# Optimization experiments

Measured on AMD Instinct MI355X. Metric: run time of the kernel, lower is better.

The kernel has to match this reference:

```python
import jax, jax.numpy as jnp
import numpy as np

N, B, C, T, IN_DIM, L, RANK, OUT_DIM = 2000, 16, 32, 12, 2, 3, 4, 1
CN = C // 4  # channel_num = 8
EPS = 1e-5


def _adj_month():
    a = np.diag(np.ones(12)) / 3.0
    np.fill_diagonal(a[1:], 1.0 / 3.0)
    np.fill_diagonal(a[:, 1:], 1.0 / 3.0)
    a[0, 11] = 1.0 / 3.0
    a[11, 0] = 1.0 / 3.0
    return jnp.asarray(a, dtype=jnp.float32)


def _circ_conv(xb, w, b, k):
    # xb: [B,N,C,T]; w: [N,CN,C,k]; b: [N,CN]  ->  [B,N,CN,T]
    # Circular pad on the right by k-1 (matches F.pad(...,(0,k-1)) mode='circular').
    Tt = xb.shape[-1]
    xp = jnp.concatenate([xb, xb[..., :k - 1]], axis=-1)          # [B,N,C,T+k-1]
    win = jnp.stack([xp[..., j:j + Tt] for j in range(k)], axis=-1)  # [B,N,C,T,k]
    return jnp.einsum('bnctk,nock->bnot', win, w) + b[None, :, :, None]


def setup_inputs() -> dict:
    key = jax.random.key(0)
    ks = jax.random.split(key, 32)

    def rn(i, shape, scale=0.05):
        return jax.random.normal(ks[i], shape, dtype=jnp.float32) * scale

    D_cw = CN * C * 18 * L   # 13824
    D_cb = CN * 4 * L        # 96
    D_rw = C * C * L         # 3072
    D_rb = C * L             # 96

    inp = jax.random.normal(ks[0], (B, IN_DIM, N, T + 1), dtype=jnp.float32)
    inp = inp.at[0, 0, 0, -1].set(5.0)  # valid month index
    adj = jax.random.uniform(ks[1], (N, N), dtype=jnp.float32) / N

    return dict(
        input=inp, adj=adj,
        characteristics=rn(2, (N, 12, RANK), 0.5),
        W_convw=rn(3, (RANK, D_cw)), b_convw=rn(4, (D_cw,)),
        W_convb=rn(5, (RANK, D_cb)), b_convb=rn(6, (D_cb,)),
        W_gatew=rn(7, (RANK, D_cw)), b_gatew=rn(8, (D_cw,)),
        W_gateb=rn(9, (RANK, D_cb)), b_gateb=rn(10, (D_cb,)),
        W_resw=rn(11, (RANK, D_rw)), b_resw=rn(12, (D_rw,)),
        W_resb=rn(13, (RANK, D_rb)), b_resb=rn(14, (D_rb,)),
        start_w=rn(15, (C, IN_DIM), 0.5), start_b=rn(16, (C,)),
        skip0_w=rn(17, (C, IN_DIM, T), 0.2), skip0_b=rn(18, (C,)),
        skip_w=rn(19, (L, C, T), 0.2), skip_b=rn(20, (L, C)),
        skipE_w=rn(21, (C, T), 0.2), skipE_b=rn(22, (C,)),
        ln_w=jnp.ones((L, C, N, T), jnp.float32),
        ln_b=jnp.zeros((L, C, N, T), jnp.float32),
        end1_w=rn(23, (C, C), 0.2), end1_b=rn(24, (C,)),
        end2_w=rn(25, (OUT_DIM, C), 0.2), end2_b=rn(26, (OUT_DIM,)),
    )


def reference(input, adj, characteristics, W_convw, b_convw, W_convb, b_convb,
              W_gatew, b_gatew, W_gateb, b_gateb, W_resw, b_resw, W_resb, b_resb,
              start_w, start_b, skip0_w, skip0_b, skip_w, skip_b, skipE_w, skipE_b,
              ln_w, ln_b, end1_w, end1_b, end2_w, end2_b):
    # month index from last time slot (eval mode: dropout = identity)
    month = jnp.mod(input[0, 0, 0, -1].astype(jnp.int32), 12)
    x_in = input[..., :T]                                   # [B,IN,N,T]

    am = _adj_month()                                       # [12,12]
    char = jnp.einsum('ms,nsr->nmr', am, characteristics)   # [N,12,R]
    char_m = jnp.take(char, month, axis=1)                  # [N,R]
    ch = adj @ char_m                                       # graph aggregation [N,R]

    cw_all = ch @ W_convw + b_convw                         # [N, CN*C*18*L]
    cb_all = ch @ W_convb + b_convb                         # [N, CN*4*L]
    gw_all = ch @ W_gatew + b_gatew
    gb_all = ch @ W_gateb + b_gateb
    rw_all = ch @ W_resw + b_resw                           # [N, C*C*L]
    rb_all = ch @ W_resb + b_resb                           # [N, C*L]

    x = jnp.einsum('bint,ci->bcnt', x_in, start_w) + start_b[None, :, None, None]
    skip = jnp.einsum('bint,cit->bcn', x_in, skip0_w) + skip0_b[None, :, None]  # [B,C,N]

    pw = CN * C                                             # 256
    # (kernel slice lo, hi, width) per multiscale branch
    slices = [(0, 2, 2), (2, 5, 3), (5, 11, 6), (11, 18, 7)]
    q = N * CN

    for i in range(L):
        residual = x
        cw = cw_all[:, i * 18 * pw:(i + 1) * 18 * pw].reshape(N, CN, C, 18)
        gw = gw_all[:, i * 18 * pw:(i + 1) * 18 * pw].reshape(N, CN, C, 18)
        # NOTE: torch flattens bias node-major THEN slices quarters -> reproduces
        # the original (node-mixing) bias indexing exactly.
        cb_flat = cb_all[:, i * 4 * CN:(i + 1) * 4 * CN].reshape(-1)   # [N*4*CN]
        gb_flat = gb_all[:, i * 4 * CN:(i + 1) * 4 * CN].reshape(-1)

        xb = jnp.transpose(x, (0, 2, 1, 3))                 # [B,N,C,T]
        f_segs, g_segs = [], []
        for s, (lo, hi, k) in enumerate(slices):
            f = _circ_conv(xb, cw[..., lo:hi], cb_flat[s * q:(s + 1) * q].reshape(N, CN), k)
            g = _circ_conv(xb, gw[..., lo:hi], gb_flat[s * q:(s + 1) * q].reshape(N, CN), k)
            f_segs.append(jnp.transpose(f, (0, 2, 1, 3)))   # [B,CN,N,T]
            g_segs.append(jnp.transpose(g, (0, 2, 1, 3)))
        filt = jnp.tanh(jnp.concatenate(f_segs, axis=1))    # [B,C,N,T]
        gate = jax.nn.sigmoid(jnp.concatenate(g_segs, axis=1))
        x = filt * gate

        s_out = jnp.einsum('bcnt,ct->bcn', x, skip_w[i]) + skip_b[i][None, :, None]
        skip = s_out + skip

        rw = rw_all[:, i * C * C:(i + 1) * C * C].reshape(N, C, C)   # [N,out,in]
        rb = rb_all[:, i * C:(i + 1) * C]                            # [N,C]
        xr = jnp.einsum('bnct,noc->bnot', jnp.transpose(x, (0, 2, 1, 3)), rw) \
             + rb[None, :, :, None]
        x = jnp.transpose(xr, (0, 2, 1, 3)) + residual

        # LayerNorm over all non-batch dims (C,N,T) with affine params
        mu = jnp.mean(x, axis=(1, 2, 3), keepdims=True)
        var = jnp.mean(jnp.square(x - mu), axis=(1, 2, 3), keepdims=True)
        x = (x - mu) / jnp.sqrt(var + EPS) * ln_w[i][None] + ln_b[i][None]

    sE = jnp.einsum('bcnt,ct->bcn', x, skipE_w) + skipE_b[None, :, None]
    skip = jax.nn.relu(sE + skip)                           # [B,C,N]
    y = jax.nn.relu(jnp.einsum('bcn,oc->bon', skip, end1_w) + end1_b[None, :, None])
    y = jnp.einsum('bcn,oc->bon', y, end2_w) + end2_b[None, :, None]
    return y[..., None]                                     # [B,OUT_DIM,N,1]
```

## Files before the change

kernel.cpp:

```cpp
#include <hip/hip_runtime.h>

#define NN 2000
#define TT 12

#define XOFF    0
#define SKOFF   6144000
#define CHOFF   7168000
#define CMOFF   7176000
#define STOFF   7184000
#define PARTOFF 7184100
#define PKWOFF  7248100
#define PKBOFF  7358692
#define PKROFF  7386340

typedef __fp16 f16x8 __attribute__((ext_vector_type(8)));
typedef __fp16 h2    __attribute__((ext_vector_type(2)));
typedef float  f32x4 __attribute__((ext_vector_type(4)));

union U32H2 { unsigned int u; __fp16 h[2]; h2 v; };
__device__ __forceinline__ unsigned int pkh(float a, float b){
  U32H2 x; x.h[0] = (__fp16)a; x.h[1] = (__fp16)b; return x.u;
}
__device__ __forceinline__ h2 u2h(unsigned int u){ U32H2 x; x.u = u; return x.v; }
__device__ __forceinline__ unsigned int h2u(h2 v){ U32H2 x; x.v = v; return x.u; }
__device__ __forceinline__ float fsig(float x){ return 1.0f/(1.0f + __expf(-x)); }
__device__ __forceinline__ float ftanh(float x){ return 1.0f - 2.0f/(1.0f + __expf(2.0f*x)); }

__global__ void k_charm(const float* __restrict__ input,
                        const float* __restrict__ charac,
                        float* __restrict__ cm)
{
  int idx = blockIdx.x*256 + threadIdx.x;
  if (idx >= NN*4) return;
  int n = idx >> 2, r = idx & 3;
  int mv = (int)input[TT];
  int m = ((mv % 12) + 12) % 12;
  int m0 = (m + 11) % 12, m2 = (m + 1) % 12;
  const float* base = charac + n*48;
  cm[idx] = (base[m0*4+r] + base[m*4+r] + base[m2*4+r]) * (1.0f/3.0f);
}

__global__ __launch_bounds__(256) void k_ch(const float* __restrict__ adj,
                                            const float* __restrict__ cm,
                                            float* __restrict__ ch)
{
  __shared__ float red[256][4];
  int n = blockIdx.x, t = threadIdx.x;
  float s0=0.f, s1=0.f, s2=0.f, s3=0.f;
  const float* arow = adj + (size_t)n*NN;
  for (int c = t; c < NN; c += 256){
    float a = arow[c];
    float4 v = *reinterpret_cast<const float4*>(cm + c*4);
    s0 = fmaf(a, v.x, s0); s1 = fmaf(a, v.y, s1);
    s2 = fmaf(a, v.z, s2); s3 = fmaf(a, v.w, s3);
  }
  red[t][0]=s0; red[t][1]=s1; red[t][2]=s2; red[t][3]=s3;
  __syncthreads();
  for (int off = 128; off > 0; off >>= 1){
    if (t < off){
      red[t][0]+=red[t+off][0]; red[t][1]+=red[t+off][1];
      red[t][2]+=red[t+off][2]; red[t][3]+=red[t+off][3];
    }
    __syncthreads();
  }
  if (t < 4) ch[n*4+t] = red[0][t];
}

__global__ __launch_bounds__(256) void k_prep(
    const float* __restrict__ Wcw, const float* __restrict__ bcw,
    const float* __restrict__ Wgw, const float* __restrict__ bgw,
    const float* __restrict__ Wrw, const float* __restrict__ brw,
    float* __restrict__ PKW, float* __restrict__ PKB, float* __restrict__ PKR)
{
  int col = blockIdx.x*256 + threadIdx.x;
  if (col < 13824){
    int layer = col / 4608;
    int i     = col - layer*4608;
    int o     = i / 576;
    int rem   = i - o*576;
    int c     = rem / 18;
    int u     = rem - c*18;
    size_t j  = (size_t)layer*4608 + o*576 + u*32 + c;
    float4 a = make_float4(Wcw[col], Wcw[13824+col], Wcw[27648+col], Wcw[41472+col]);
    float4 b = make_float4(Wgw[col], Wgw[13824+col], Wgw[27648+col], Wgw[41472+col]);
    *reinterpret_cast<float4*>(PKW + j*8)     = a;
    *reinterpret_cast<float4*>(PKW + j*8 + 4) = b;
    *reinterpret_cast<float2*>(PKB + j*2) = make_float2(bcw[col], bgw[col]);
  }
  if (col < 3072){
    float4 r = make_float4(Wrw[col], Wrw[3072+col], Wrw[6144+col], Wrw[9216+col]);
    *reinterpret_cast<float4*>(PKR + (size_t)col*8) = r;
    PKR[(size_t)col*8 + 4] = brw[col];
  }
}

__global__ __launch_bounds__(256) void k_stats(
    int layer, const float* __restrict__ parts, float* __restrict__ stats)
{
  __shared__ float red[256];
  const int j = blockIdx.x, tid = threadIdx.x;
  float s = 0.f;
  for (int i = tid; i < NN; i += 256) s += parts[(size_t)i*32 + j];
  red[tid] = s;
  __syncthreads();
  for (int off = 128; off > 0; off >>= 1){
    if (tid < off) red[tid] += red[tid+off];
    __syncthreads();
  }
  if (tid == 0) stats[layer*32 + j] = red[0];
}

__global__ __launch_bounds__(256,3) void k_layer(
    int layer,
    __fp16* __restrict__ xbuf, float* __restrict__ skipbuf,
    const float* __restrict__ ch, const float* __restrict__ stats,
    float* __restrict__ parts,
    const float* __restrict__ input,
    const float* __restrict__ PKW, const float* __restrict__ PKB,
    const float* __restrict__ PKR,
    const float* __restrict__ Wcb, const float* __restrict__ bcb,
    const float* __restrict__ Wgb, const float* __restrict__ bgb,
    const float* __restrict__ Wrb, const float* __restrict__ brb,
    const float* __restrict__ start_w, const float* __restrict__ start_b,
    const float* __restrict__ sk0w, const float* __restrict__ sk0b,
    const float* __restrict__ skw_all, const float* __restrict__ skb_all,
    const float* __restrict__ lnw_all, const float* __restrict__ lnb_all)
{
  __shared__ __fp16 AhG[10752];
  __shared__ __fp16 xh[7680];
  __shared__ __fp16 rwh[1280];
  __shared__ float skred[1024];
  __shared__ float wred[128];
  __shared__ float ubuf[1280];
  __shared__ float skwv[384];
  __shared__ float skbv[32], fbias[32], gbias[32], rbv[32];
  __shared__ float muv[16], rsv[16];

  const int tid = threadIdx.x;
  const int n = blockIdx.x;

  float* swv  = ubuf;
  float* sbv  = ubuf + 64;
  float* s0wv = ubuf + 96;
  float* s0bv = ubuf + 864;
  float* xin  = ubuf + 896;
  __fp16* lnh = reinterpret_cast<__fp16*>(ubuf);

  const float c0v = ch[n*4+0], c1v = ch[n*4+1], c2v = ch[n*4+2], c3v = ch[n*4+3];

  for (int i = tid; i < 32; i += 256) skbv[i] = skb_all[layer*32+i];
  for (int i = tid; i < 384; i += 256) skwv[i] = skw_all[layer*384+i];
  if (layer == 0){
    for (int i = tid; i < 64; i += 256) swv[i] = start_w[i];
    for (int i = tid; i < 32; i += 256){ sbv[i] = start_b[i]; s0bv[i] = sk0b[i]; }
    for (int i = tid; i < 768; i += 256) s0wv[i] = sk0w[i];
    for (int i = tid; i < 384; i += 256){
      int bb = i/24, r = i%24, d = r/12, t = r%12;
      xin[i] = input[(((size_t)bb*2 + d)*NN + n)*13 + t];
    }
  } else {
    for (int i = tid; i < 384; i += 256){
      int c = i/12, t = i%12;
      size_t o = (((size_t)(layer-1)*32 + c)*NN + n)*12 + t;
      lnh[t*32+c]       = (__fp16)lnw_all[o];
      lnh[384 + t*32+c] = (__fp16)lnb_all[o];
    }
    if (tid < 16){
      float S1 = stats[(layer-1)*32 + tid];
      float S2 = stats[(layer-1)*32 + 16 + tid];
      const float M = 768000.0f;
      float mu = S1 / M;
      muv[tid] = mu;
      rsv[tid] = rsqrtf(S2/M - mu*mu + 1e-5f);
    }
  }

  {
    const int cc = tid & 31;
    const int o  = tid >> 5;
    const int o104 = o*104, o232 = o*232;
    const float* pw  = PKW + (size_t)layer*4608*8 + ((size_t)o*576 + cc)*8;
    const float* pbp = PKB + (size_t)layer*4608*2 + ((size_t)o*576 + cc)*2;
#pragma unroll
    for (int u = 0; u < 18; ++u){
      const int s    = (u >= 2) + (u >= 5) + (u >= 11);
      const int lo   = (s == 0) ? 0 : ((s == 1) ? 2 : ((s == 2) ? 5 : 11));
      const int jj   = u - lo;
      const int strd = (s >= 2) ? 232 : 104;
      const int base = ((s >= 2) ? 3328 : 0) + ((s & 1) << 3)*strd + jj*32;
      const int ooff = (s >= 2) ? o232 : o104;
      float4 pwf = *reinterpret_cast<const float4*>(pw + (size_t)u*256);
      float4 pwg = *reinterpret_cast<const float4*>(pw + (size_t)u*256 + 4);
      float2 pb  = *reinterpret_cast<const float2*>(pbp + (size_t)u*64);
      float wf = fmaf(c0v, pwf.x, fmaf(c1v, pwf.y,
                 fmaf(c2v, pwf.z, fmaf(c3v, pwf.w, pb.x))));
      float wg = fmaf(c0v, pwg.x, fmaf(c1v, pwg.y,
                 fmaf(c2v, pwg.z, fmaf(c3v, pwg.w, pb.y))));
      AhG[base + ooff + cc]             = (__fp16)wf;
      AhG[base + ooff + cc + 16*strd]   = (__fp16)wg;
    }
  }
  for (int i = tid; i < 1024; i += 256){
    int grp = i >> 8, rem = i & 255, r = rem >> 5, c = rem & 31;
    int base = (grp < 2) ? 0 : 3328;
    int strd = (grp < 2) ? 104 : 232;
    int off  = (grp < 2) ? 64 : 192;
    int gofs = (grp & 1) ? 16*strd : 0;
    AhG[base + gofs + r*strd + off + c] = (__fp16)0.f;
  }
  for (int i = tid; i < 1024; i += 256){
    int col = layer*1024 + i;
    float4 pr = *reinterpret_cast<const float4*>(PKR + (size_t)col*8);
    float rb = PKR[(size_t)col*8 + 4];
    float v = fmaf(c0v, pr.x, fmaf(c1v, pr.y,
              fmaf(c2v, pr.z, fmaf(c3v, pr.w, rb))));
    rwh[(i>>5)*40 + (i&31)] = (__fp16)v;
  }
  if (tid < 32){
    int oc = tid;
    int s = oc >> 3;
    int v = ((n&3)<<3) + (oc&7);
    int col = layer*32 + v;
    float cb0 = ch[(s*500 + (n>>2))*4 + 0];
    float cb1 = ch[(s*500 + (n>>2))*4 + 1];
    float cb2 = ch[(s*500 + (n>>2))*4 + 2];
    float cb3 = ch[(s*500 + (n>>2))*4 + 3];
    fbias[oc] = fmaf(cb0, Wcb[col], fmaf(cb1, Wcb[96+col],
                fmaf(cb2, Wcb[192+col], fmaf(cb3, Wcb[288+col], bcb[col]))));
    gbias[oc] = fmaf(cb0, Wgb[col], fmaf(cb1, Wgb[96+col],
                fmaf(cb2, Wgb[192+col], fmaf(cb3, Wgb[288+col], bgb[col]))));
    int colr = layer*32 + oc;
    rbv[oc] = fmaf(c0v, Wrb[colr], fmaf(c1v, Wrb[96+colr],
              fmaf(c2v, Wrb[192+colr], fmaf(c3v, Wrb[288+colr], brb[colr]))));
  }
  __syncthreads();

  if (tid < 192){
    int b = tid & 15, t = tid >> 4;
    unsigned int pk[16];
    if (layer == 0){
      float xa = xin[b*24 + t], xb2 = xin[b*24 + 12 + t];
      float xv[32];
#pragma unroll
      for (int c = 0; c < 32; ++c)
        xv[c] = fmaf(swv[c*2], xa, fmaf(swv[c*2+1], xb2, sbv[c]));
#pragma unroll
      for (int j = 0; j < 16; ++j) pk[j] = pkh(xv[2*j], xv[2*j+1]);
    } else {
      const uint4* src = reinterpret_cast<const uint4*>(
          xbuf + (((size_t)b*NN + n)*12 + t)*32);
      uint4 u0 = src[0], u1 = src[1], u2 = src[2], u3 = src[3];
      unsigned int uu[16] = {u0.x,u0.y,u0.z,u0.w, u1.x,u1.y,u1.z,u1.w,
                             u2.x,u2.y,u2.z,u2.w, u3.x,u3.y,u3.z,u3.w};
      __fp16 muh = (__fp16)muv[b], rsh = (__fp16)rsv[b];
      h2 mu2; mu2.x = muh; mu2.y = muh;
      h2 rs2; rs2.x = rsh; rs2.y = rsh;
      const h2* lnw2 = reinterpret_cast<const h2*>(lnh + t*32);
      const h2* lnb2 = reinterpret_cast<const h2*>(lnh + 384 + t*32);
#pragma unroll
      for (int j = 0; j < 16; ++j){
        h2 v = u2h(uu[j]);
        h2 r = (v - mu2) * rs2;
        h2 x2 = r * lnw2[j] + lnb2[j];
        pk[j] = h2u(x2);
      }
    }
    uint4* dst = reinterpret_cast<uint4*>(&xh[(t*16 + b)*40]);
    dst[0] = make_uint4(pk[0], pk[1], pk[2], pk[3]);
    dst[1] = make_uint4(pk[4], pk[5], pk[6], pk[7]);
    dst[2] = make_uint4(pk[8], pk[9], pk[10], pk[11]);
    dst[3] = make_uint4(pk[12],pk[13],pk[14],pk[15]);
  }
  __syncthreads();

  const int lane = tid & 63, w = tid >> 6;
  const int h = w & 1, nh = w >> 1;
  const int r16 = lane & 15, hi4 = lane >> 4;
  const int c0 = hi4*8;
  const int oc0 = h*16 + hi4*4;

  const __fp16* Ab = AhG + (h ? 3328 : 0);
  const int As  = h ? 232 : 104;
  const int njj = h ? 7 : 3;
  f16x8 aF[7], aG[7];
#pragma unroll 7
  for (int jj = 0; jj < 7; ++jj) if (jj < njj){
    aF[jj] = *reinterpret_cast<const f16x8*>(&Ab[r16*As + jj*32 + c0]);
    aG[jj] = *reinterpret_cast<const f16x8*>(&Ab[(16 + r16)*As + jj*32 + c0]);
  }
  f16x8 ar = *reinterpret_cast<const f16x8*>(&rwh[(h*16 + r16)*40 + c0]);
  float fb4[4], gb4[4], rb4[4];
#pragma unroll
  for (int i2 = 0; i2 < 4; ++i2){
    fb4[i2] = fbias[oc0+i2]; gb4[i2] = gbias[oc0+i2]; rb4[i2] = rbv[oc0+i2];
  }
  __syncthreads();
  __fp16* gh = AhG;

  float sv[4] = {0.f, 0.f, 0.f, 0.f};
#pragma unroll
  for (int q = 0; q < 6; ++q){
    int nt = nh*6 + q;
    f32x4 accf = {0.f,0.f,0.f,0.f}, accg = {0.f,0.f,0.f,0.f};
#pragma unroll 7
    for (int jj = 0; jj < 7; ++jj) if (jj < njj){
      int tp = nt + jj; if (tp >= 12) tp -= 12;
      f16x8 bf = *reinterpret_cast<const f16x8*>(&xh[(tp*16 + r16)*40 + c0]);
      accf = __builtin_amdgcn_mfma_f32_16x16x32_f16(aF[jj], bf, accf, 0, 0, 0);
      accg = __builtin_amdgcn_mfma_f32_16x16x32_f16(aG[jj], bf, accg, 0, 0, 0);
    }
    float gv4[4];
#pragma unroll
    for (int i2 = 0; i2 < 4; ++i2){
      float fv = ftanh(accf[i2] + fb4[i2]);
      float gg = fsig(accg[i2] + gb4[i2]);
      gv4[i2] = fv * gg;
      sv[i2] = fmaf(gv4[i2], skwv[(oc0+i2)*12 + nt], sv[i2]);
    }
    *reinterpret_cast<uint2*>(&gh[(nt*16 + r16)*40 + oc0]) =
        make_uint2(pkh(gv4[0], gv4[1]), pkh(gv4[2], gv4[3]));
  }
#pragma unroll
  for (int i2 = 0; i2 < 4; ++i2)
    skred[((oc0+i2)*16 + r16)*2 + nh] = sv[i2];
  __syncthreads();

  for (int e = tid; e < 512; e += 256){
    int b = e >> 5, oc = e & 31;
    float sk = skred[(oc*16+b)*2] + skred[(oc*16+b)*2+1] + skbv[oc];
    size_t so = ((size_t)b*NN + n)*32 + oc;
    if (layer == 0){
      float s0 = s0bv[oc];
#pragma unroll
      for (int r = 0; r < 24; ++r) s0 = fmaf(xin[b*24+r], s0wv[oc*24+r], s0);
      skipbuf[so] = sk + s0;
    } else {
      skipbuf[so] += sk;
    }
  }
  {
    float s1 = 0.f, s2 = 0.f;
#pragma unroll
    for (int q = 0; q < 6; ++q){
      int nt = nh*6 + q;
      f16x8 bg = *reinterpret_cast<const f16x8*>(&gh[(nt*16 + r16)*40 + c0]);
      f32x4 z = {0.f,0.f,0.f,0.f};
      f32x4 acc = __builtin_amdgcn_mfma_f32_16x16x32_f16(ar, bg, z, 0, 0, 0);
      uint2 xu = *reinterpret_cast<const uint2*>(&xh[(nt*16 + r16)*40 + oc0]);
      U32H2 ua, ub; ua.u = xu.x; ub.u = xu.y;
      float o0 = acc[0] + rb4[0] + (float)ua.h[0];
      float o1 = acc[1] + rb4[1] + (float)ua.h[1];
      float o2 = acc[2] + rb4[2] + (float)ub.h[0];
      float o3 = acc[3] + rb4[3] + (float)ub.h[1];
      *reinterpret_cast<uint2*>(
          xbuf + (((size_t)r16*NN + n)*12 + nt)*32 + oc0) =
          make_uint2(pkh(o0, o1), pkh(o2, o3));
      s1 += o0 + o1 + o2 + o3;
      s2 = fmaf(o0,o0, fmaf(o1,o1, fmaf(o2,o2, fmaf(o3,o3, s2))));
    }
    s1 += __shfl_xor(s1, 16); s2 += __shfl_xor(s2, 16);
    s1 += __shfl_xor(s1, 32); s2 += __shfl_xor(s2, 32);
    if (hi4 == 0){
      wred[(w*16 + r16)*2]     = s1;
      wred[(w*16 + r16)*2 + 1] = s2;
    }
  }
  __syncthreads();
  if (tid < 16){
    float a1 = 0.f, a2 = 0.f;
    for (int w2 = 0; w2 < 4; ++w2){
      a1 += wred[(w2*16 + tid)*2];
      a2 += wred[(w2*16 + tid)*2 + 1];
    }
    parts[(size_t)n*32 + tid]      = a1;
    parts[(size_t)n*32 + 16 + tid] = a2;
  }
}

__global__ __launch_bounds__(256) void k_final(
    const __fp16* __restrict__ xbuf, const float* __restrict__ skipbuf,
    const float* __restrict__ stats,
    const float* __restrict__ lnw_all, const float* __restrict__ lnb_all,
    const float* __restrict__ skEw, const float* __restrict__ skEb,
    const float* __restrict__ e1w, const float* __restrict__ e1b,
    const float* __restrict__ e2w, const float* __restrict__ e2b,
    float* __restrict__ out)
{
  __shared__ float lnw[384], lnb[384], skE[384];
  __shared__ float e1[32*33];
  __shared__ float e1bv[32], e2v[32], skEbv[32];
  __shared__ float muv[16], rsv[16];
  __shared__ float skf[8][33];
  const int tid = threadIdx.x, n = blockIdx.x;
  for (int i = tid; i < 384; i += 256){
    int c = i/12, t = i%12;
    size_t o = (((size_t)2*32 + c)*NN + n)*12 + t;
    lnw[i] = lnw_all[o]; lnb[i] = lnb_all[o];
    skE[i] = skEw[i];
  }
  for (int i = tid; i < 1024; i += 256) e1[(i>>5)*33 + (i&31)] = e1w[i];
  if (tid < 32){ e1bv[tid] = e1b[tid]; e2v[tid] = e2w[tid]; skEbv[tid] = skEb[tid]; }
  if (tid < 16){
    float S1 = stats[64+tid], S2 = stats[80+tid];
    const float M = 768000.0f;
    float mu = S1/M; muv[tid] = mu;
    rsv[tid] = rsqrtf(S2/M - mu*mu + 1e-5f);
  }
  __syncthreads();
  const float e2b0 = e2b[0];
  for (int bo = 0; bo < 2; ++bo){
    const int g = tid >> 5, c = tid & 31, b = bo*8 + g;
    float xr[12];
#pragma unroll
    for (int t = 0; t < 12; ++t)
      xr[t] = (float)xbuf[(((size_t)b*NN + n)*12 + t)*32 + c];
    const float mu = muv[b], rs = rsv[b];
    float se = 0.0f;
#pragma unroll
    for (int t = 0; t < 12; ++t){
      float xv = fmaf((xr[t]-mu)*rs, lnw[c*12+t], lnb[c*12+t]);
      se = fmaf(xv, skE[c*12+t], se);
    }
    float sk = se + skEbv[c] + skipbuf[((size_t)b*NN+n)*32 + c];
    skf[g][c] = fmaxf(sk, 0.0f);
    __syncthreads();
    float acc = e1bv[c];
#pragma unroll
    for (int cc = 0; cc < 32; ++cc) acc = fmaf(skf[g][cc], e1[c*33+cc], acc);
    float y1 = fmaxf(acc, 0.0f);
    float part = y1 * e2v[c];
#pragma unroll
    for (int off = 16; off > 0; off >>= 1) part += __shfl_down(part, off, 32);
    if (c == 0) out[(size_t)b*NN + n] = part + e2b0;
    __syncthreads();
  }
}

extern "C" void kernel_launch(void* const* d_in, const int* in_sizes, int n_in,
                              void* d_out, int out_size, void* d_ws, size_t ws_size,
                              hipStream_t stream)
{
  (void)in_sizes; (void)n_in; (void)out_size; (void)ws_size;
  const float* input   = (const float*)d_in[0];
  const float* adj     = (const float*)d_in[1];
  const float* charac  = (const float*)d_in[2];
  const float* Wcw     = (const float*)d_in[3];
  const float* bcw     = (const float*)d_in[4];
  const float* Wcb     = (const float*)d_in[5];
  const float* bcb     = (const float*)d_in[6];
  const float* Wgw     = (const float*)d_in[7];
  const float* bgw     = (const float*)d_in[8];
  const float* Wgb     = (const float*)d_in[9];
  const float* bgb     = (const float*)d_in[10];
  const float* Wrw     = (const float*)d_in[11];
  const float* brw     = (const float*)d_in[12];
  const float* Wrb     = (const float*)d_in[13];
  const float* brb     = (const float*)d_in[14];
  const float* start_w = (const float*)d_in[15];
  const float* start_b = (const float*)d_in[16];
  const float* sk0w    = (const float*)d_in[17];
  const float* sk0b    = (const float*)d_in[18];
  const float* skw     = (const float*)d_in[19];
  const float* skb     = (const float*)d_in[20];
  const float* skEw    = (const float*)d_in[21];
  const float* skEb    = (const float*)d_in[22];
  const float* lnw     = (const float*)d_in[23];
  const float* lnb     = (const float*)d_in[24];
  const float* e1w     = (const float*)d_in[25];
  const float* e1b     = (const float*)d_in[26];
  const float* e2w     = (const float*)d_in[27];
  const float* e2b     = (const float*)d_in[28];

  float* ws     = (float*)d_ws;
  __fp16* xbuf  = (__fp16*)(ws + XOFF);
  float* skipb  = ws + SKOFF;
  float* chbuf  = ws + CHOFF;
  float* cmbuf  = ws + CMOFF;
  float* stats  = ws + STOFF;
  float* parts  = ws + PARTOFF;
  float* PKW    = ws + PKWOFF;
  float* PKB    = ws + PKBOFF;
  float* PKR    = ws + PKROFF;
  float* outp   = (float*)d_out;

  k_prep<<<54, 256, 0, stream>>>(Wcw, bcw, Wgw, bgw, Wrw, brw, PKW, PKB, PKR);
  k_charm<<<32, 256, 0, stream>>>(input, charac, cmbuf);
  k_ch<<<NN, 256, 0, stream>>>(adj, cmbuf, chbuf);
  for (int layer = 0; layer < 3; ++layer){
    k_layer<<<NN, 256, 0, stream>>>(layer, xbuf, skipb, chbuf, stats, parts, input,
        PKW, PKB, PKR, Wcb, bcb, Wgb, bgb, Wrb, brb,
        start_w, start_b, sk0w, sk0b, skw, skb, lnw, lnb);
    k_stats<<<32, 256, 0, stream>>>(layer, parts, stats);
  }
  k_final<<<NN, 256, 0, stream>>>(xbuf, skipb, stats, lnw, lnb,
      skEw, skEb, e1w, e1b, e2w, e2b, outp);
}
```

Measured before the change: 192.2 us.

## Shrink k_layer LDS footprint and template on layer 0 for higher occupancy

Templates k_layer on whether it is layer 0, so layers 1-2 use a smaller shared buffer and a launch bound of 4 blocks per CU instead of 3. LDS is cut further by storing skip weights, biases and skip partial sums as fp16, aliasing skip-reduction and wred scratch into the AhG buffer, and tightening the xh/gh row pitch from 40 to 36 halves with 8-byte loads. The goal is more resident blocks per CU to hide latency. The trade-offs are extra fp16 rounding on biases and skip sums, possible LDS bank conflicts from the new pitch, and narrower loads.

```diff
diff --git a/kernel.cpp b/kernel.cpp
--- a/kernel.cpp
+++ b/kernel.cpp
@@ -18,6 +18,7 @@
 typedef float  f32x4 __attribute__((ext_vector_type(4)));
 
 union U32H2 { unsigned int u; __fp16 h[2]; h2 v; };
+union U2X8  { struct { uint2 a, b; } p; f16x8 v; };
 __device__ __forceinline__ unsigned int pkh(float a, float b){
   U32H2 x; x.h[0] = (__fp16)a; x.h[1] = (__fp16)b; return x.u;
 }
@@ -110,7 +111,8 @@
   if (tid == 0) stats[layer*32 + j] = red[0];
 }
 
-__global__ __launch_bounds__(256,3) void k_layer(
+template<int IS_L0>
+__global__ __launch_bounds__(256, IS_L0 ? 3 : 4) void k_layer(
     int layer,
     __fp16* __restrict__ xbuf, float* __restrict__ skipbuf,
     const float* __restrict__ ch, const float* __restrict__ stats,
@@ -127,14 +129,11 @@
     const float* __restrict__ lnw_all, const float* __restrict__ lnb_all)
 {
   __shared__ __fp16 AhG[10752];
-  __shared__ __fp16 xh[7680];
+  __shared__ __fp16 xh[6912];
   __shared__ __fp16 rwh[1280];
-  __shared__ float skred[1024];
-  __shared__ float wred[128];
-  __shared__ float ubuf[1280];
-  __shared__ float skwv[384];
-  __shared__ float skbv[32], fbias[32], gbias[32], rbv[32];
-  __shared__ float muv[16], rsv[16];
+  __shared__ __fp16 skwv_h[384];
+  __shared__ __fp16 bias_h[128];
+  __shared__ float  ubuf[IS_L0 ? 1280 : 384];
 
   const int tid = threadIdx.x;
   const int n = blockIdx.x;
@@ -148,9 +147,9 @@
 
   const float c0v = ch[n*4+0], c1v = ch[n*4+1], c2v = ch[n*4+2], c3v = ch[n*4+3];
 
-  for (int i = tid; i < 32; i += 256) skbv[i] = skb_all[layer*32+i];
-  for (int i = tid; i < 384; i += 256) skwv[i] = skw_all[layer*384+i];
-  if (layer == 0){
+  for (int i = tid; i < 32; i += 256) bias_h[96+i] = (__fp16)skb_all[layer*32+i];
+  for (int i = tid; i < 384; i += 256) skwv_h[i] = (__fp16)skw_all[layer*384+i];
+  if (IS_L0){
     for (int i = tid; i < 64; i += 256) swv[i] = start_w[i];
     for (int i = tid; i < 32; i += 256){ sbv[i] = start_b[i]; s0bv[i] = sk0b[i]; }
     for (int i = tid; i < 768; i += 256) s0wv[i] = sk0w[i];
@@ -164,14 +163,6 @@
       size_t o = (((size_t)(layer-1)*32 + c)*NN + n)*12 + t;
       lnh[t*32+c]       = (__fp16)lnw_all[o];
       lnh[384 + t*32+c] = (__fp16)lnb_all[o];
-    }
-    if (tid < 16){
-      float S1 = stats[(layer-1)*32 + tid];
-      float S2 = stats[(layer-1)*32 + 16 + tid];
-      const float M = 768000.0f;
-      float mu = S1 / M;
-      muv[tid] = mu;
-      rsv[tid] = rsqrtf(S2/M - mu*mu + 1e-5f);
     }
   }
 
@@ -225,20 +216,20 @@
     float cb1 = ch[(s*500 + (n>>2))*4 + 1];
     float cb2 = ch[(s*500 + (n>>2))*4 + 2];
     float cb3 = ch[(s*500 + (n>>2))*4 + 3];
-    fbias[oc] = fmaf(cb0, Wcb[col], fmaf(cb1, Wcb[96+col],
-                fmaf(cb2, Wcb[192+col], fmaf(cb3, Wcb[288+col], bcb[col]))));
-    gbias[oc] = fmaf(cb0, Wgb[col], fmaf(cb1, Wgb[96+col],
-                fmaf(cb2, Wgb[192+col], fmaf(cb3, Wgb[288+col], bgb[col]))));
+    bias_h[oc] = (__fp16)fmaf(cb0, Wcb[col], fmaf(cb1, Wcb[96+col],
+                 fmaf(cb2, Wcb[192+col], fmaf(cb3, Wcb[288+col], bcb[col]))));
+    bias_h[32+oc] = (__fp16)fmaf(cb0, Wgb[col], fmaf(cb1, Wgb[96+col],
+                 fmaf(cb2, Wgb[192+col], fmaf(cb3, Wgb[288+col], bgb[col]))));
     int colr = layer*32 + oc;
-    rbv[oc] = fmaf(c0v, Wrb[colr], fmaf(c1v, Wrb[96+colr],
-              fmaf(c2v, Wrb[192+colr], fmaf(c3v, Wrb[288+colr], brb[colr]))));
+    bias_h[64+oc] = (__fp16)fmaf(c0v, Wrb[colr], fmaf(c1v, Wrb[96+colr],
+                 fmaf(c2v, Wrb[192+colr], fmaf(c3v, Wrb[288+colr], brb[colr]))));
   }
   __syncthreads();
 
   if (tid < 192){
     int b = tid & 15, t = tid >> 4;
     unsigned int pk[16];
-    if (layer == 0){
+    if (IS_L0){
       float xa = xin[b*24 + t], xb2 = xin[b*24 + 12 + t];
       float xv[32];
 #pragma unroll
@@ -252,7 +243,12 @@
       uint4 u0 = src[0], u1 = src[1], u2 = src[2], u3 = src[3];
       unsigned int uu[16] = {u0.x,u0.y,u0.z,u0.w, u1.x,u1.y,u1.z,u1.w,
                              u2.x,u2.y,u2.z,u2.w, u3.x,u3.y,u3.z,u3.w};
-      __fp16 muh = (__fp16)muv[b], rsh = (__fp16)rsv[b];
+      const float M = 768000.0f;
+      float S1 = stats[(layer-1)*32 + b];
+      float S2 = stats[(layer-1)*32 + 16 + b];
+      float muf = S1 / M;
+      float rsf = rsqrtf(S2/M - muf*muf + 1e-5f);
+      __fp16 muh = (__fp16)muf, rsh = (__fp16)rsf;
       h2 mu2; mu2.x = muh; mu2.y = muh;
       h2 rs2; rs2.x = rsh; rs2.y = rsh;
       const h2* lnw2 = reinterpret_cast<const h2*>(lnh + t*32);
@@ -265,11 +261,9 @@
         pk[j] = h2u(x2);
       }
     }
-    uint4* dst = reinterpret_cast<uint4*>(&xh[(t*16 + b)*40]);
-    dst[0] = make_uint4(pk[0], pk[1], pk[2], pk[3]);
-    dst[1] = make_uint4(pk[4], pk[5], pk[6], pk[7]);
-    dst[2] = make_uint4(pk[8], pk[9], pk[10], pk[11]);
-    dst[3] = make_uint4(pk[12],pk[13],pk[14],pk[15]);
+    uint2* dst = reinterpret_cast<uint2*>(&xh[(t*16 + b)*36]);
+#pragma unroll
+    for (int j = 0; j < 8; ++j) dst[j] = make_uint2(pk[2*j], pk[2*j+1]);
   }
   __syncthreads();
 
@@ -292,10 +286,14 @@
   float fb4[4], gb4[4], rb4[4];
 #pragma unroll
   for (int i2 = 0; i2 < 4; ++i2){
-    fb4[i2] = fbias[oc0+i2]; gb4[i2] = gbias[oc0+i2]; rb4[i2] = rbv[oc0+i2];
-  }
-  __syncthreads();
-  __fp16* gh = AhG;
+    fb4[i2] = (float)bias_h[oc0+i2];
+    gb4[i2] = (float)bias_h[32+oc0+i2];
+    rb4[i2] = (float)bias_h[64+oc0+i2];
+  }
+  __syncthreads();
+  __fp16* gh  = AhG;
+  __fp16* skh = AhG + 6912;
+  float*  wred = reinterpret_cast<float*>(AhG + 7936);
 
   float sv[4] = {0.f, 0.f, 0.f, 0.f};
 #pragma unroll
@@ -305,9 +303,10 @@
 #pragma unroll 7
     for (int jj = 0; jj < 7; ++jj) if (jj < njj){
       int tp = nt + jj; if (tp >= 12) tp -= 12;
-      f16x8 bf = *reinterpret_cast<const f16x8*>(&xh[(tp*16 + r16)*40 + c0]);
-      accf = __builtin_amdgcn_mfma_f32_16x16x32_f16(aF[jj], bf, accf, 0, 0, 0);
-      accg = __builtin_amdgcn_mfma_f32_16x16x32_f16(aG[jj], bf, accg, 0, 0, 0);
+      const uint2* xp = reinterpret_cast<const uint2*>(&xh[(tp*16 + r16)*36 + c0]);
+      U2X8 bf; bf.p.a = xp[0]; bf.p.b = xp[1];
+      accf = __builtin_amdgcn_mfma_f32_16x16x32_f16(aF[jj], bf.v, accf, 0, 0, 0);
+      accg = __builtin_amdgcn_mfma_f32_16x16x32_f16(aG[jj], bf.v, accg, 0, 0, 0);
     }
     float gv4[4];
 #pragma unroll
@@ -315,21 +314,22 @@
       float fv = ftanh(accf[i2] + fb4[i2]);
       float gg = fsig(accg[i2] + gb4[i2]);
       gv4[i2] = fv * gg;
-      sv[i2] = fmaf(gv4[i2], skwv[(oc0+i2)*12 + nt], sv[i2]);
-    }
-    *reinterpret_cast<uint2*>(&gh[(nt*16 + r16)*40 + oc0]) =
+      sv[i2] = fmaf(gv4[i2], (float)skwv_h[(oc0+i2)*12 + nt], sv[i2]);
+    }
+    *reinterpret_cast<uint2*>(&gh[(nt*16 + r16)*36 + oc0]) =
         make_uint2(pkh(gv4[0], gv4[1]), pkh(gv4[2], gv4[3]));
   }
 #pragma unroll
   for (int i2 = 0; i2 < 4; ++i2)
-    skred[((oc0+i2)*16 + r16)*2 + nh] = sv[i2];
+    skh[((oc0+i2)*16 + r16)*2 + nh] = (__fp16)sv[i2];
   __syncthreads();
 
   for (int e = tid; e < 512; e += 256){
     int b = e >> 5, oc = e & 31;
-    float sk = skred[(oc*16+b)*2] + skred[(oc*16+b)*2+1] + skbv[oc];
+    float sk = (float)skh[(oc*16+b)*2] + (float)skh[(oc*16+b)*2+1]
+             + (float)bias_h[96+oc];
     size_t so = ((size_t)b*NN + n)*32 + oc;
-    if (layer == 0){
+    if (IS_L0){
       float s0 = s0bv[oc];
 #pragma unroll
       for (int r = 0; r < 24; ++r) s0 = fmaf(xin[b*24+r], s0wv[oc*24+r], s0);
@@ -343,10 +343,11 @@
 #pragma unroll
     for (int q = 0; q < 6; ++q){
       int nt = nh*6 + q;
-      f16x8 bg = *reinterpret_cast<const f16x8*>(&gh[(nt*16 + r16)*40 + c0]);
+      const uint2* gp = reinterpret_cast<const uint2*>(&gh[(nt*16 + r16)*36 + c0]);
+      U2X8 bg; bg.p.a = gp[0]; bg.p.b = gp[1];
       f32x4 z = {0.f,0.f,0.f,0.f};
-      f32x4 acc = __builtin_amdgcn_mfma_f32_16x16x32_f16(ar, bg, z, 0, 0, 0);
-      uint2 xu = *reinterpret_cast<const uint2*>(&xh[(nt*16 + r16)*40 + oc0]);
+      f32x4 acc = __builtin_amdgcn_mfma_f32_16x16x32_f16(ar, bg.v, z, 0, 0, 0);
+      uint2 xu = *reinterpret_cast<const uint2*>(&xh[(nt*16 + r16)*36 + oc0]);
       U32H2 ua, ub; ua.u = xu.x; ub.u = xu.y;
       float o0 = acc[0] + rb4[0] + (float)ua.h[0];
       float o1 = acc[1] + rb4[1] + (float)ua.h[1];
@@ -486,8 +487,12 @@
   k_prep<<<54, 256, 0, stream>>>(Wcw, bcw, Wgw, bgw, Wrw, brw, PKW, PKB, PKR);
   k_charm<<<32, 256, 0, stream>>>(input, charac, cmbuf);
   k_ch<<<NN, 256, 0, stream>>>(adj, cmbuf, chbuf);
-  for (int layer = 0; layer < 3; ++layer){
-    k_layer<<<NN, 256, 0, stream>>>(layer, xbuf, skipb, chbuf, stats, parts, input,
+  k_layer<1><<<NN, 256, 0, stream>>>(0, xbuf, skipb, chbuf, stats, parts, input,
+      PKW, PKB, PKR, Wcb, bcb, Wgb, bgb, Wrb, brb,
+      start_w, start_b, sk0w, sk0b, skw, skb, lnw, lnb);
+  k_stats<<<32, 256, 0, stream>>>(0, parts, stats);
+  for (int layer = 1; layer < 3; ++layer){
+    k_layer<0><<<NN, 256, 0, stream>>>(layer, xbuf, skipb, chbuf, stats, parts, input,
         PKW, PKB, PKR, Wcb, bcb, Wgb, bgb, Wrb, brb,
         start_w, start_b, sk0w, sk0b, skw, skb, lnw, lnb);
     k_stats<<<32, 256, 0, stream>>>(layer, parts, stats);
```

Result: slower. 202.3 us (+5.3%).
